# Kernel optimization log

Measured on AMD Instinct MI355X. Metric: run time of the kernel, lower is better.

## Reference

```python
import jax, jax.numpy as jnp
import numpy as np

WS = 5   # window_size
VN = 8   # view_num -> H = W = VN*WS = 40


def _layernorm(x, g, b, eps=1e-5):
    mu = x.mean(-1, keepdims=True)
    var = ((x - mu) ** 2).mean(-1, keepdims=True)
    return (x - mu) * jax.lax.rsqrt(var + eps) * g + b


def _rel_index():
    # standard Swin relative-position index for a WS x WS window
    coords = np.stack(np.meshgrid(np.arange(WS), np.arange(WS), indexing='ij')).reshape(2, -1)
    rel = (coords[:, :, None] - coords[:, None, :]).transpose(1, 2, 0)  # (T,T,2)
    rel = rel + (WS - 1)
    return rel[:, :, 0] * (2 * WS - 1) + rel[:, :, 1]  # (T,T) int


def _attn_mask(H, W):
    # checkerboard mask: outer product of flattened per-window checkerboard,
    # 0 where both positions are 'on', -100 elsewhere (matches masked_fill logic)
    ckbd = np.zeros((H, W), np.float32)
    ckbd[0::2, 1::2] = 1.0
    ckbd[1::2, 0::2] = 1.0
    win = ckbd.reshape(VN, WS, VN, WS).transpose(0, 2, 1, 3).reshape(VN * VN, WS * WS)
    m = win[:, :, None] * win[:, None, :]  # (N,T,T)
    return np.where(m == 0.0, -100.0, 0.0).astype(np.float32)


def setup_inputs() -> dict:
    key = jax.random.key(0)
    ks = jax.random.split(key, 8)
    B, C, H, W = 64, 256, 40, 40
    nh = 8
    dim2 = 2 * C
    hid = int(dim2 * 2.0)

    def n(k, shape, s=0.02):
        return jax.random.normal(k, shape, jnp.float32) * s

    return dict(
        x=jax.random.normal(ks[0], (B, C, H, W), jnp.float32),
        qkv_w=n(ks[1], (C, 3 * C)), qkv_b=jnp.zeros((3 * C,), jnp.float32),
        rel_table=n(ks[2], ((2 * WS - 1) ** 2, nh)),
        proj_w=n(ks[3], (C, dim2)), proj_b=jnp.zeros((dim2,), jnp.float32),
        mlp_w1=n(ks[4], (dim2, hid)), mlp_b1=jnp.zeros((hid,), jnp.float32),
        mlp_w2=n(ks[5], (hid, dim2)), mlp_b2=jnp.zeros((dim2,), jnp.float32),
        norm1_g=jnp.ones((C,), jnp.float32), norm1_b=jnp.zeros((C,), jnp.float32),
        norm2_g=jnp.ones((dim2,), jnp.float32), norm2_b=jnp.zeros((dim2,), jnp.float32),
    )


def reference(x, qkv_w, qkv_b, rel_table, proj_w, proj_b,
              mlp_w1, mlp_b1, mlp_w2, mlp_b2,
              norm1_g, norm1_b, norm2_g, norm2_b):
    B, C, H, W = x.shape
    nh = rel_table.shape[1]
    hd = C // nh
    N = VN * VN           # windows
    T = WS * WS           # tokens per window
    scale = hd ** -0.5

    xs = _layernorm(x.reshape(B, C, H * W).transpose(0, 2, 1), norm1_g, norm1_b)  # (B,L,C)
    qkv = xs @ qkv_w + qkv_b                                   # (B,L,3C)
    qkv = qkv.reshape(B, H, W, 3, C).transpose(3, 0, 4, 1, 2)  # (3,B,C,H,W)
    # windowize: (3,B,C,u,ws,v,ws) -> (3,B,N,C,T)
    qkv = qkv.reshape(3, B, C, VN, WS, VN, WS).transpose(0, 1, 3, 5, 2, 4, 6).reshape(3, B, N, C, T)
    # NOTE: original splits C as (head_dim, num_heads) -- head index is MINOR
    qkv = qkv.reshape(3, B, N, hd, nh, T).transpose(0, 1, 2, 4, 5, 3)  # (3,B,N,nh,T,hd)
    q, k, v = qkv[0] * scale, qkv[1], qkv[2]

    attn = jnp.einsum('bnhtd,bnhsd->bnhts', q, k)              # (B,N,nh,T,T)
    bias = rel_table[jnp.asarray(_rel_index())].transpose(2, 0, 1)  # (nh,T,T)
    mask = jnp.asarray(_attn_mask(H, W))                       # (N,T,T)
    attn = jax.nn.softmax(attn + bias[None, None] + mask[None, :, None], axis=-1)

    out = jnp.einsum('bnhts,bnhsd->bnhtd', attn, v)            # (B,N,nh,T,hd)
    out = out.reshape(B, N, nh, WS, WS, hd).transpose(0, 1, 3, 4, 2, 5)  # (B,N,ws,ws,nh,hd)
    # 'B (u v) h w nh c -> B (u h v w) (nh c)'
    out = out.reshape(B, VN, VN, WS, WS, C).transpose(0, 1, 3, 2, 4, 5).reshape(B, H * W, C)

    y = out @ proj_w + proj_b                                  # (B,L,2C)
    h = _layernorm(y, norm2_g, norm2_b)
    h = jax.nn.gelu(h @ mlp_w1 + mlp_b1, approximate=False) @ mlp_w2 + mlp_b2
    y = y + h
    return y.transpose(0, 2, 1).reshape(B, -1, H, W)           # (B,2C,H,W)
```

## Files before the change

### kernel.cpp

```cpp
#include <hip/hip_runtime.h>
#include <math.h>

#define B_   64
#define C_   256
#define L_   1600
#define T_   25
#define ROWS (B_*L_)
#define QSCALE 0.17677669529663687f

typedef _Float16 f16;
typedef f16 f16x8 __attribute__((ext_vector_type(8)));
typedef f16 f16x4 __attribute__((ext_vector_type(4)));
typedef f16 f16x2 __attribute__((ext_vector_type(2)));
typedef float f32x4 __attribute__((ext_vector_type(4)));

__device__ __forceinline__ void gload_lds16(const void* g, void* l) {
  __builtin_amdgcn_global_load_lds(
      (const __attribute__((address_space(1))) unsigned int*)g,
      (__attribute__((address_space(3))) unsigned int*)l, 16, 0, 0);
}

__device__ __forceinline__ float dot8(f16x8 a, f16x8 b, float acc) {
  union U { f16x8 v; f16x2 p[4]; };
  U ua; ua.v = a;
  U ub; ub.v = b;
#pragma unroll
  for (int i = 0; i < 4; ++i)
    acc = __builtin_amdgcn_fdot2(ua.p[i], ub.p[i], acc, false);
  return acc;
}

__global__ __launch_bounds__(256) void wtrans(const float* __restrict__ w,
                                              f16* __restrict__ o, int K, int N) {
  __shared__ f16 tile[64][72];
  int tid = threadIdx.x;
  int n0 = blockIdx.x * 64, k0 = blockIdx.y * 64;
  int nn = tid & 63, kq = tid >> 6;
#pragma unroll
  for (int i = 0; i < 16; ++i) {
    int k = kq * 16 + i;
    tile[nn][k] = (f16)w[(size_t)(k0 + k) * N + n0 + nn];
  }
  __syncthreads();
#pragma unroll
  for (int jj = 0; jj < 2; ++jj) {
    int e = jj * 256 + tid;
    int nr = e >> 3, kb = e & 7;
    *(f16x8*)&o[(size_t)(n0 + nr) * K + k0 + kb * 8] = *(const f16x8*)&tile[nr][kb * 8];
  }
}

__global__ __launch_bounds__(256) void ln1_fused(const float* __restrict__ x,
    const float* __restrict__ g, const float* __restrict__ be,
    f16* __restrict__ xs) {
  __shared__ float t32[256][65];
  __shared__ float gL[256], beL[256];
  int tid = threadIdx.x;
  gL[tid] = g[tid]; beL[tid] = be[tid];
  int r0 = blockIdx.x * 64;
  int w = tid >> 6, rl = tid & 63;
  int grow = r0 + rl;
  int b = grow / L_, l = grow - b * L_;
  const float* xb = x + (size_t)b * (C_ * L_) + l;
#pragma unroll
  for (int i = 0; i < 64; ++i) {
    int c = w + i * 4;
    t32[c][rl] = xb[(size_t)c * L_];
  }
  __syncthreads();
  int row = tid >> 2, q = tid & 3;
  float s = 0.f, s2 = 0.f;
#pragma unroll
  for (int i = 0; i < 64; ++i) {
    float vv = t32[q * 64 + i][row];
    s += vv; s2 += vv * vv;
  }
  s += __shfl_xor(s, 1); s2 += __shfl_xor(s2, 1);
  s += __shfl_xor(s, 2); s2 += __shfl_xor(s2, 2);
  float m = s * (1.0f / 256.0f);
  float rr = rsqrtf(s2 * (1.0f / 256.0f) - m * m + 1e-5f);
  f16* orow = &xs[(size_t)(r0 + row) * 256 + q * 64];
#pragma unroll
  for (int z8 = 0; z8 < 8; ++z8) {
    f16x8 ov;
#pragma unroll
    for (int z = 0; z < 8; ++z) {
      int c = q * 64 + z8 * 8 + z;
      ov[z] = (f16)((t32[c][row] - m) * rr * gL[c] + beL[c]);
    }
    *(f16x8*)(orow + z8 * 8) = ov;
  }
}

template<int K, int N, int EPI, int NCB>
__global__ __launch_bounds__(512) void gemm16(
    const f16* __restrict__ A, const f16* __restrict__ BT,
    const float* __restrict__ bias,
    float* __restrict__ outF, f16* __restrict__ outH,
    const f16* __restrict__ resid, int row_off, int nrp8) {
  __shared__ __align__(16) char smem[(EPI == 3) ? 64 * 129 * 4 : 16384];
  f16* As = (f16*)smem;
  f16* Bs = (f16*)(smem + 8192);
  float* tT = (float*)smem;
  int tid = threadIdx.x;
  int w = tid >> 6, lane = tid & 63;
  int wr = w >> 2, wc = w & 3;
  int bid = blockIdx.x;
  int xcd = bid & 7, j1d = bid >> 3;
  int member = j1d % NCB, grp = j1d / NCB;
  int r0 = (xcd * nrp8 + grp) * 128;
  int n0 = member * 128;

  f32x4 acc[4][2] = {};
  int srow = tid >> 2, st = tid & 3;
  int scb = st ^ ((srow >> 1) & 3);

  for (int k0 = 0; k0 < K; k0 += 32) {
    gload_lds16(A + (size_t)(r0 + srow) * K + k0 + scb * 8, &As[w * 512]);
    gload_lds16(BT + (size_t)(n0 + srow) * K + k0 + scb * 8, &Bs[w * 512]);
    __syncthreads();

    f16x8 af[4], bf[2];
#pragma unroll
    for (int m = 0; m < 4; ++m) {
      int ar = wr * 64 + m * 16 + (lane & 15);
      int sl = (lane >> 4) ^ ((ar >> 1) & 3);
      af[m] = *(const f16x8*)&As[ar * 32 + sl * 8];
    }
#pragma unroll
    for (int n = 0; n < 2; ++n) {
      int br = wc * 32 + n * 16 + (lane & 15);
      int sl = (lane >> 4) ^ ((br >> 1) & 3);
      bf[n] = *(const f16x8*)&Bs[br * 32 + sl * 8];
    }
#pragma unroll
    for (int m = 0; m < 4; ++m)
#pragma unroll
      for (int n = 0; n < 2; ++n)
        acc[m][n] = __builtin_amdgcn_mfma_f32_16x16x32_f16(af[m], bf[n], acc[m][n], 0, 0, 0);
    __syncthreads();
  }

  if constexpr (EPI != 3) {
#pragma unroll
    for (int m = 0; m < 4; ++m) {
#pragma unroll
      for (int n = 0; n < 2; ++n) {
        int gcol = n0 + wc * 32 + n * 16 + (lane & 15);
        float bb = bias[gcol];
#pragma unroll
        for (int j2 = 0; j2 < 4; ++j2) {
          int grow = r0 + wr * 64 + m * 16 + ((lane >> 4) << 2) + j2;
          float vv = acc[m][n][j2] + bb;
          if constexpr (EPI == 0) {
            outH[(size_t)grow * N + gcol] = (f16)vv;
          } else {
            float gl = 0.5f * vv * (1.0f + erff(vv * 0.70710678118654752f));
            outH[(size_t)grow * N + gcol] = (f16)gl;
          }
        }
      }
    }
  } else {
    for (int p = 0; p < 2; ++p) {
      if (wr == p) {
#pragma unroll
        for (int m = 0; m < 4; ++m) {
          int lr = m * 16 + ((lane >> 4) << 2);
#pragma unroll
          for (int n = 0; n < 2; ++n) {
            int lc = wc * 32 + n * 16 + (lane & 15);
            int gcol = n0 + lc;
            float bb = bias[gcol];
#pragma unroll
            for (int j2 = 0; j2 < 4; ++j2) {
              int grow = row_off + r0 + p * 64 + lr + j2;
              tT[(lr + j2) * 129 + lc] =
                  acc[m][n][j2] + bb + (float)resid[(size_t)grow * 512 + gcol];
            }
          }
        }
      }
      __syncthreads();
#pragma unroll
      for (int it = 0; it < 4; ++it) {
        int idx = it * 512 + tid;
        int col = idx >> 4;
        int r4 = idx & 15;
        int grow0 = row_off + r0 + p * 64 + r4 * 4;
        int b = grow0 / L_;
        int l = grow0 - b * L_;
        float4 o = make_float4(tT[(r4 * 4 + 0) * 129 + col],
                               tT[(r4 * 4 + 1) * 129 + col],
                               tT[(r4 * 4 + 2) * 129 + col],
                               tT[(r4 * 4 + 3) * 129 + col]);
        *(float4*)&outF[((size_t)b * 512 + n0 + col) * L_ + l] = o;
      }
      __syncthreads();
    }
  }
}

#define PST 776
__global__ __launch_bounds__(256) void attn_kernel(const f16* __restrict__ qkv,
                                                   const float* __restrict__ rel,
                                                   f16* __restrict__ outp) {
  __shared__ f16 qc[T_][PST];
  __shared__ f16 relL[81 * 8];
  int tid = threadIdx.x;
  int bn = blockIdx.x;
  int b = bn >> 6, n = bn & 63;
  int u = n >> 3, v = n & 7;

  for (int e = tid; e < 648; e += 256) relL[e] = (f16)rel[e];

  for (int e = tid; e < T_ * 96; e += 256) {
    int t = e / 96;
    int g = e - t * 96;
    int i = t / 5, j = t - i * 5;
    int l = (u * 5 + i) * 40 + v * 5 + j;
    f16x8 val = *(const f16x8*)&qkv[(size_t)(b * L_ + l) * 768 + g * 8];
    int which = g >> 5;
    int d = g & 31;
    int base = which * 256 + d;
#pragma unroll
    for (int h = 0; h < 8; ++h)
      qc[t][base + h * 32] = val[h];
  }
  __syncthreads();

  int h = tid >> 5, t = tid & 31;
  if (t < T_) {
    int i1 = t / 5, j1 = t - i1 * 5;
    int par1 = (u + v + i1 + j1) & 1;
    const f16* qp = &qc[t][h * 32];
    f16x8 q0 = *(const f16x8*)(qp + 0);
    f16x8 q1 = *(const f16x8*)(qp + 8);
    f16x8 q2 = *(const f16x8*)(qp + 16);
    f16x8 q3 = *(const f16x8*)(qp + 24);

    float p[T_];
    float mx = -1e30f;
#pragma unroll
    for (int s = 0; s < T_; ++s) {
      int i2 = s / 5, j2 = s - i2 * 5;
      const f16* kp = &qc[s][256 + h * 32];
      f16x8 k0 = *(const f16x8*)(kp + 0);
      f16x8 k1 = *(const f16x8*)(kp + 8);
      f16x8 k2 = *(const f16x8*)(kp + 16);
      f16x8 k3 = *(const f16x8*)(kp + 24);
      float d0 = 0.f, d1 = 0.f;
      d0 = dot8(q0, k0, d0);
      d1 = dot8(q1, k1, d1);
      d0 = dot8(q2, k2, d0);
      d1 = dot8(q3, k3, d1);
      float bias = (float)relL[((i1 - i2 + 4) * 9 + (j1 - j2 + 4)) * 8 + h];
      int par2 = (u + v + i2 + j2) & 1;
      float sc = (d0 + d1) * QSCALE + bias + ((par1 & par2) ? 0.0f : -100.0f);
      p[s] = sc;
      mx = fmaxf(mx, sc);
    }
    float sum = 0.f;
#pragma unroll
    for (int s = 0; s < T_; ++s) {
      float e = __expf(p[s] - mx);
      p[s] = e;
      sum += e;
    }
    float inv = 1.0f / sum;
#pragma unroll
    for (int s = 0; s < T_; ++s) p[s] *= inv;

    int l = (u * 5 + i1) * 40 + v * 5 + j1;
    f16* op = &outp[(size_t)(b * L_ + l) * 256 + h * 32];

#pragma unroll
    for (int half = 0; half < 2; ++half) {
      float acc[16] = {};
#pragma unroll
      for (int s = 0; s < T_; ++s) {
        const f16* vp = &qc[s][512 + h * 32 + half * 16];
        f16x8 v0 = *(const f16x8*)(vp + 0);
        f16x8 v1 = *(const f16x8*)(vp + 8);
        float ps = p[s];
#pragma unroll
        for (int z = 0; z < 8; ++z) {
          acc[z]     += ps * (float)v0[z];
          acc[8 + z] += ps * (float)v1[z];
        }
      }
#pragma unroll
      for (int z8 = 0; z8 < 2; ++z8) {
        f16x8 ov;
#pragma unroll
        for (int z = 0; z < 8; ++z) ov[z] = (f16)acc[z8 * 8 + z];
        *(f16x8*)(op + half * 16 + z8 * 8) = ov;
      }
    }
  }
}

__global__ __launch_bounds__(256) void ln2_fused(const f16* __restrict__ y,
    const float* __restrict__ g, const float* __restrict__ be,
    f16* __restrict__ yln) {
  int wv = threadIdx.x >> 6, lane = threadIdx.x & 63;
  int row = blockIdx.x * 4 + wv;
  const f16x8* yp = (const f16x8*)(y + (size_t)row * 512);
  f16x8 h0 = yp[lane];
  float v[8];
  float s = 0.f, s2 = 0.f;
#pragma unroll
  for (int z = 0; z < 8; ++z) {
    v[z] = (float)h0[z];
    s += v[z]; s2 += v[z] * v[z];
  }
#pragma unroll
  for (int o = 32; o; o >>= 1) { s += __shfl_xor(s, o); s2 += __shfl_xor(s2, o); }
  float m = s * (1.0f / 512.0f);
  float rr = rsqrtf(s2 * (1.0f / 512.0f) - m * m + 1e-5f);
  float4 g0 = ((const float4*)g)[lane * 2], g1 = ((const float4*)g)[lane * 2 + 1];
  float4 b0 = ((const float4*)be)[lane * 2], b1 = ((const float4*)be)[lane * 2 + 1];
  float gg[8] = {g0.x, g0.y, g0.z, g0.w, g1.x, g1.y, g1.z, g1.w};
  float bb[8] = {b0.x, b0.y, b0.z, b0.w, b1.x, b1.y, b1.z, b1.w};
  f16x8 o8;
#pragma unroll
  for (int z = 0; z < 8; ++z)
    o8[z] = (f16)((v[z] - m) * rr * gg[z] + bb[z]);
  *(f16x8*)&yln[(size_t)row * 512 + lane * 8] = o8;
}

extern "C" void kernel_launch(void* const* d_in, const int* in_sizes, int n_in,
                              void* d_out, int out_size, void* d_ws, size_t ws_size,
                              hipStream_t stream) {
  const float* x      = (const float*)d_in[0];
  const float* qkv_w  = (const float*)d_in[1];
  const float* qkv_b  = (const float*)d_in[2];
  const float* rel    = (const float*)d_in[3];
  const float* proj_w = (const float*)d_in[4];
  const float* proj_b = (const float*)d_in[5];
  const float* w1     = (const float*)d_in[6];
  const float* b1     = (const float*)d_in[7];
  const float* w2     = (const float*)d_in[8];
  const float* b2     = (const float*)d_in[9];
  const float* g1     = (const float*)d_in[10];
  const float* be1    = (const float*)d_in[11];
  const float* g2     = (const float*)d_in[12];
  const float* be2    = (const float*)d_in[13];
  float* out = (float*)d_out;

  char* w8 = (char*)d_ws;
  f16* qkv_wT  = (f16*)(w8 + 1638400);
  f16* proj_wT = qkv_wT + 768 * 256;
  f16* w1T     = proj_wT + 512 * 256;
  f16* w2T     = w1T + 1024 * 512;
  char* P0 = w8 + 4390912;
  f16* qkv_h = (f16*)P0;
  f16* y_h   = (f16*)P0;
  char* P1 = P0 + (size_t)ROWS * 768 * 2;
  f16* xs_h  = (f16*)P1;
  f16* att_h = (f16*)(P1 + (size_t)ROWS * 256 * 2);
  f16* yln   = (f16*)P1;
  char* P2 = P1 + (size_t)ROWS * 512 * 2;
  f16* hid = (f16*)P2;

  size_t need_full = 4390912 + (size_t)ROWS * 768 * 2 + (size_t)ROWS * 512 * 2
                   + (size_t)ROWS * 1024 * 2;
  bool full = ws_size >= need_full;

  wtrans<<<dim3(768 / 64, 256 / 64), 256, 0, stream>>>(qkv_w, qkv_wT, 256, 768);
  wtrans<<<dim3(512 / 64, 256 / 64), 256, 0, stream>>>(proj_w, proj_wT, 256, 512);
  wtrans<<<dim3(1024 / 64, 512 / 64), 256, 0, stream>>>(w1, w1T, 512, 1024);
  wtrans<<<dim3(512 / 64, 1024 / 64), 256, 0, stream>>>(w2, w2T, 1024, 512);

  ln1_fused<<<ROWS / 64, 256, 0, stream>>>(x, g1, be1, xs_h);

  gemm16<256, 768, 0, 6><<<6 * (ROWS / 128), 512, 0, stream>>>(
      xs_h, qkv_wT, qkv_b, nullptr, qkv_h, nullptr, 0, (ROWS / 128) / 8);

  attn_kernel<<<B_ * 64, 256, 0, stream>>>(qkv_h, rel, att_h);

  gemm16<256, 512, 0, 4><<<4 * (ROWS / 128), 512, 0, stream>>>(
      att_h, proj_wT, proj_b, nullptr, y_h, nullptr, 0, (ROWS / 128) / 8);

  ln2_fused<<<ROWS / 4, 256, 0, stream>>>(y_h, g2, be2, yln);

  if (full) {
    gemm16<512, 1024, 2, 8><<<8 * (ROWS / 128), 512, 0, stream>>>(
        yln, w1T, b1, nullptr, hid, nullptr, 0, (ROWS / 128) / 8);
    gemm16<1024, 512, 3, 4><<<4 * (ROWS / 128), 512, 0, stream>>>(
        hid, w2T, b2, out, nullptr, y_h, 0, (ROWS / 128) / 8);
  } else {
    const int CHUNK = ROWS / 4;
    for (int c = 0; c < 4; ++c) {
      int off = c * CHUNK;
      gemm16<512, 1024, 2, 8><<<8 * (CHUNK / 128), 512, 0, stream>>>(
          yln + (size_t)off * 512, w1T, b1, nullptr, hid, nullptr, off, (CHUNK / 128) / 8);
      gemm16<1024, 512, 3, 4><<<4 * (CHUNK / 128), 512, 0, stream>>>(
          hid, w2T, b2, out, nullptr, y_h, off, (CHUNK / 128) / 8);
    }
  }
  (void)in_sizes; (void)n_in; (void)out_size;
}
```

Measured before the change: 745.2 us.

## Double-buffer GEMM LDS tiles with 4 waves and larger per-wave tiles

Rewrites the shared f16 MFMA GEMM to use 256 threads (4 waves, each computing a 64x64 sub-tile) instead of 8 waves of 64x32. The global-to-LDS loads go into a double buffer, so the next K-tile is fetched while the current one is computed, with one barrier per iteration instead of two. The transposed-output epilogue now writes float4 directly from registers, dropping the LDS transpose stage. This raises register pressure and lowers wave-level parallelism per block. The direct residual reads and strided output stores may also be less coalesced.

```diff
diff --git a/kernel.cpp b/kernel.cpp
--- a/kernel.cpp
+++ b/kernel.cpp
@@ -93,65 +93,101 @@
 }
 
 template<int K, int N, int EPI, int NCB>
-__global__ __launch_bounds__(512) void gemm16(
+__global__ __launch_bounds__(256) void gemm16(
     const f16* __restrict__ A, const f16* __restrict__ BT,
     const float* __restrict__ bias,
     float* __restrict__ outF, f16* __restrict__ outH,
     const f16* __restrict__ resid, int row_off, int nrp8) {
-  __shared__ __align__(16) char smem[(EPI == 3) ? 64 * 129 * 4 : 16384];
-  f16* As = (f16*)smem;
-  f16* Bs = (f16*)(smem + 8192);
-  float* tT = (float*)smem;
+  __shared__ f16 As[2][128 * 32];
+  __shared__ f16 Bs[2][128 * 32];
   int tid = threadIdx.x;
   int w = tid >> 6, lane = tid & 63;
-  int wr = w >> 2, wc = w & 3;
+  int wr = w >> 1, wc = w & 1;
   int bid = blockIdx.x;
   int xcd = bid & 7, j1d = bid >> 3;
   int member = j1d % NCB, grp = j1d / NCB;
   int r0 = (xcd * nrp8 + grp) * 128;
   int n0 = member * 128;
 
-  f32x4 acc[4][2] = {};
-  int srow = tid >> 2, st = tid & 3;
-  int scb = st ^ ((srow >> 1) & 3);
-
-  for (int k0 = 0; k0 < K; k0 += 32) {
-    gload_lds16(A + (size_t)(r0 + srow) * K + k0 + scb * 8, &As[w * 512]);
-    gload_lds16(BT + (size_t)(n0 + srow) * K + k0 + scb * 8, &Bs[w * 512]);
-    __syncthreads();
-
-    f16x8 af[4], bf[2];
+  f32x4 acc[4][4] = {};
+
+  int srow0 = w * 16 + (lane >> 2);
+  int st4 = lane & 3;
+
+  const int NT = K / 32;
+
+#define STAGE_T(kt, buf)                                                      \
+  {                                                                           \
+    int k0s = (kt) * 32;                                                      \
+    _Pragma("unroll")                                                         \
+    for (int i = 0; i < 2; ++i) {                                             \
+      int row = i * 64 + srow0;                                               \
+      int cb = st4 ^ ((row >> 1) & 3);                                        \
+      gload_lds16(A + (size_t)(r0 + row) * K + k0s + cb * 8,                  \
+                  &As[buf][(i * 4 + w) * 512]);                               \
+    }                                                                         \
+    _Pragma("unroll")                                                         \
+    for (int i = 0; i < 2; ++i) {                                             \
+      int row = i * 64 + srow0;                                               \
+      int cb = st4 ^ ((row >> 1) & 3);                                        \
+      gload_lds16(BT + (size_t)(n0 + row) * K + k0s + cb * 8,                 \
+                  &Bs[buf][(i * 4 + w) * 512]);                               \
+    }                                                                         \
+  }
+
+#define COMPUTE_T(buf)                                                        \
+  {                                                                           \
+    f16x8 af[4], bf[4];                                                       \
+    _Pragma("unroll")                                                         \
+    for (int m = 0; m < 4; ++m) {                                             \
+      int ar = wr * 64 + m * 16 + (lane & 15);                                \
+      int sl = (lane >> 4) ^ ((ar >> 1) & 3);                                 \
+      af[m] = *(const f16x8*)&As[buf][ar * 32 + sl * 8];                      \
+    }                                                                         \
+    _Pragma("unroll")                                                         \
+    for (int n = 0; n < 4; ++n) {                                             \
+      int br = wc * 64 + n * 16 + (lane & 15);                                \
+      int sl = (lane >> 4) ^ ((br >> 1) & 3);                                 \
+      bf[n] = *(const f16x8*)&Bs[buf][br * 32 + sl * 8];                      \
+    }                                                                         \
+    _Pragma("unroll")                                                         \
+    for (int m = 0; m < 4; ++m)                                               \
+      _Pragma("unroll")                                                       \
+      for (int n = 0; n < 4; ++n)                                             \
+        acc[m][n] =                                                           \
+            __builtin_amdgcn_mfma_f32_16x16x32_f16(af[m], bf[n], acc[m][n],   \
+                                                   0, 0, 0);                  \
+  }
+
+  STAGE_T(0, 0);
+  asm volatile("s_waitcnt vmcnt(0)" ::: "memory");
+  __builtin_amdgcn_s_barrier();
+
+  int cur = 0;
+#pragma unroll 2
+  for (int t = 0; t < NT - 1; ++t) {
+    STAGE_T(t + 1, cur ^ 1);
+    COMPUTE_T(cur);
+    asm volatile("s_waitcnt vmcnt(0) lgkmcnt(0)" ::: "memory");
+    __builtin_amdgcn_s_barrier();
+    cur ^= 1;
+  }
+  COMPUTE_T(cur);
+
+#undef STAGE_T
+#undef COMPUTE_T
+
+  if constexpr (EPI != 3) {
 #pragma unroll
     for (int m = 0; m < 4; ++m) {
-      int ar = wr * 64 + m * 16 + (lane & 15);
-      int sl = (lane >> 4) ^ ((ar >> 1) & 3);
-      af[m] = *(const f16x8*)&As[ar * 32 + sl * 8];
-    }
-#pragma unroll
-    for (int n = 0; n < 2; ++n) {
-      int br = wc * 32 + n * 16 + (lane & 15);
-      int sl = (lane >> 4) ^ ((br >> 1) & 3);
-      bf[n] = *(const f16x8*)&Bs[br * 32 + sl * 8];
-    }
-#pragma unroll
-    for (int m = 0; m < 4; ++m)
-#pragma unroll
-      for (int n = 0; n < 2; ++n)
-        acc[m][n] = __builtin_amdgcn_mfma_f32_16x16x32_f16(af[m], bf[n], acc[m][n], 0, 0, 0);
-    __syncthreads();
-  }
-
-  if constexpr (EPI != 3) {
-#pragma unroll
-    for (int m = 0; m < 4; ++m) {
-#pragma unroll
-      for (int n = 0; n < 2; ++n) {
-        int gcol = n0 + wc * 32 + n * 16 + (lane & 15);
+#pragma unroll
+      for (int n = 0; n < 4; ++n) {
+        int gcol = n0 + wc * 64 + n * 16 + (lane & 15);
         float bb = bias[gcol];
 #pragma unroll
-        for (int j2 = 0; j2 < 4; ++j2) {
-          int grow = r0 + wr * 64 + m * 16 + ((lane >> 4) << 2) + j2;
-          float vv = acc[m][n][j2] + bb;
+        for (int j = 0; j < 4; ++j) {
+          int grow = r0 + wr * 64 + m * 16 + ((lane >> 4) << 2) + j;
+          float vv = acc[m][n][j] + bb;
           if constexpr (EPI == 0) {
             outH[(size_t)grow * N + gcol] = (f16)vv;
           } else {
@@ -162,41 +198,23 @@
       }
     }
   } else {
-    for (int p = 0; p < 2; ++p) {
-      if (wr == p) {
-#pragma unroll
-        for (int m = 0; m < 4; ++m) {
-          int lr = m * 16 + ((lane >> 4) << 2);
-#pragma unroll
-          for (int n = 0; n < 2; ++n) {
-            int lc = wc * 32 + n * 16 + (lane & 15);
-            int gcol = n0 + lc;
-            float bb = bias[gcol];
-#pragma unroll
-            for (int j2 = 0; j2 < 4; ++j2) {
-              int grow = row_off + r0 + p * 64 + lr + j2;
-              tT[(lr + j2) * 129 + lc] =
-                  acc[m][n][j2] + bb + (float)resid[(size_t)grow * 512 + gcol];
-            }
-          }
-        }
+#pragma unroll
+    for (int m = 0; m < 4; ++m) {
+      int growl = r0 + wr * 64 + m * 16 + ((lane >> 4) << 2);
+      int growg = row_off + growl;
+      int b = growg / L_;
+      int l = growg - b * L_;
+#pragma unroll
+      for (int n = 0; n < 4; ++n) {
+        int gcol = n0 + wc * 64 + n * 16 + (lane & 15);
+        float bb = bias[gcol];
+        float4 o;
+        o.x = acc[m][n][0] + bb + (float)resid[(size_t)(growg + 0) * 512 + gcol];
+        o.y = acc[m][n][1] + bb + (float)resid[(size_t)(growg + 1) * 512 + gcol];
+        o.z = acc[m][n][2] + bb + (float)resid[(size_t)(growg + 2) * 512 + gcol];
+        o.w = acc[m][n][3] + bb + (float)resid[(size_t)(growg + 3) * 512 + gcol];
+        *(float4*)&outF[((size_t)b * 512 + gcol) * L_ + l] = o;
       }
-      __syncthreads();
-#pragma unroll
-      for (int it = 0; it < 4; ++it) {
-        int idx = it * 512 + tid;
-        int col = idx >> 4;
-        int r4 = idx & 15;
-        int grow0 = row_off + r0 + p * 64 + r4 * 4;
-        int b = grow0 / L_;
-        int l = grow0 - b * L_;
-        float4 o = make_float4(tT[(r4 * 4 + 0) * 129 + col],
-                               tT[(r4 * 4 + 1) * 129 + col],
-                               tT[(r4 * 4 + 2) * 129 + col],
-                               tT[(r4 * 4 + 3) * 129 + col]);
-        *(float4*)&outF[((size_t)b * 512 + n0 + col) * L_ + l] = o;
-      }
-      __syncthreads();
     }
   }
 }
@@ -374,28 +392,28 @@
 
   ln1_fused<<<ROWS / 64, 256, 0, stream>>>(x, g1, be1, xs_h);
 
-  gemm16<256, 768, 0, 6><<<6 * (ROWS / 128), 512, 0, stream>>>(
+  gemm16<256, 768, 0, 6><<<6 * (ROWS / 128), 256, 0, stream>>>(
       xs_h, qkv_wT, qkv_b, nullptr, qkv_h, nullptr, 0, (ROWS / 128) / 8);
 
   attn_kernel<<<B_ * 64, 256, 0, stream>>>(qkv_h, rel, att_h);
 
-  gemm16<256, 512, 0, 4><<<4 * (ROWS / 128), 512, 0, stream>>>(
+  gemm16<256, 512, 0, 4><<<4 * (ROWS / 128), 256, 0, stream>>>(
       att_h, proj_wT, proj_b, nullptr, y_h, nullptr, 0, (ROWS / 128) / 8);
 
   ln2_fused<<<ROWS / 4, 256, 0, stream>>>(y_h, g2, be2, yln);
 
   if (full) {
-    gemm16<512, 1024, 2, 8><<<8 * (ROWS / 128), 512, 0, stream>>>(
+    gemm16<512, 1024, 2, 8><<<8 * (ROWS / 128), 256, 0, stream>>>(
         yln, w1T, b1, nullptr, hid, nullptr, 0, (ROWS / 128) / 8);
-    gemm16<1024, 512, 3, 4><<<4 * (ROWS / 128), 512, 0, stream>>>(
+    gemm16<1024, 512, 3, 4><<<4 * (ROWS / 128), 256, 0, stream>>>(
         hid, w2T, b2, out, nullptr, y_h, 0, (ROWS / 128) / 8);
   } else {
     const int CHUNK = ROWS / 4;
     for (int c = 0; c < 4; ++c) {
       int off = c * CHUNK;
-      gemm16<512, 1024, 2, 8><<<8 * (CHUNK / 128), 512, 0, stream>>>(
+      gemm16<512, 1024, 2, 8><<<8 * (CHUNK / 128), 256, 0, stream>>>(
           yln + (size_t)off * 512, w1T, b1, nullptr, hid, nullptr, off, (CHUNK / 128) / 8);
-      gemm16<1024, 512, 3, 4><<<4 * (CHUNK / 128), 512, 0, stream>>>(
+      gemm16<1024, 512, 3, 4><<<4 * (CHUNK / 128), 256, 0, stream>>>(
           hid, w2T, b2, out, nullptr, y_h, off, (CHUNK / 128) / 8);
     }
   }
```

Measured after the change: 767.2 us. +2.9%, slower.
